# Performance work log

Hardware: AMD Instinct MI355X
Metric: run time of the kernel (lower is better)

Reference implementation:

```python
import jax, jax.numpy as jnp
import numpy as np

B, T, C, H, K = 4, 2048, 2048, 32, 64
CHUNK = 64  # matches `splits = 64` in the torch source
EPS = 0.00064


def setup_inputs() -> dict:
    key = jax.random.key(0)
    ks = jax.random.split(key, 16)
    return {
        "x": jax.random.normal(ks[0], (B, T, C), jnp.float32),
        "state": jax.random.normal(ks[1], (1, 1, C), jnp.float32) * 0.1,
        "wkvstate": jax.random.normal(ks[2], (H, K, K), jnp.float32) * 0.02,
        "time_mix_k": jax.random.uniform(ks[3], (1, 1, C), jnp.float32),
        "time_mix_v": jax.random.uniform(ks[4], (1, 1, C), jnp.float32),
        "time_mix_r": jax.random.uniform(ks[5], (1, 1, C), jnp.float32),
        "time_mix_g": jax.random.uniform(ks[6], (1, 1, C), jnp.float32),
        "time_decay": jax.random.normal(ks[7], (H, K), jnp.float32) * 0.5,
        "time_faaaa": jax.random.normal(ks[8], (H, K), jnp.float32) * 0.1,
        "w_r": jax.random.normal(ks[9], (C, C), jnp.float32) * 0.02,
        "w_k": jax.random.normal(ks[10], (C, C), jnp.float32) * 0.02,
        "w_v": jax.random.normal(ks[11], (C, C), jnp.float32) * 0.02,
        "w_g": jax.random.normal(ks[12], (C, C), jnp.float32) * 0.02,
        "w_o": jax.random.normal(ks[13], (C, C), jnp.float32) * 0.02,
        "ln_w": jnp.ones((C,), jnp.float32),
        "ln_b": jnp.zeros((C,), jnp.float32),
    }


def reference(x, state, wkvstate, time_mix_k, time_mix_v, time_mix_r, time_mix_g,
              time_decay, time_faaaa, w_r, w_k, w_v, w_g, w_o, ln_w, ln_b):
    Bx, Tx, Cx = x.shape
    Hx, Kx = time_decay.shape

    # TimeShift (training path): prepend learned state, drop last token
    xx = jnp.concatenate([jnp.broadcast_to(state, (Bx, 1, Cx)), x[:, :-1]], axis=1)
    xk = x * time_mix_k + xx * (1.0 - time_mix_k)
    xv = x * time_mix_v + xx * (1.0 - time_mix_v)
    xr = x * time_mix_r + xx * (1.0 - time_mix_r)
    xg = x * time_mix_g + xx * (1.0 - time_mix_g)

    g = jax.nn.silu(xg @ w_g.T)  # (B,T,C)

    def to_heads(t):  # (B,T,C) -> (B,H,T,K)
        return t.reshape(Bx, Tx, Hx, Kx).transpose(0, 2, 1, 3)

    r = to_heads(xr @ w_r.T)
    k = to_heads(xk @ w_k.T)
    v = to_heads(xv @ w_v.T)

    w = jnp.exp(-jnp.exp(time_decay))  # (H,K), per-channel decay in (0,1)
    t_idx = jnp.arange(Tx)
    wfor = w[None, :, None, :] ** t_idx[None, None, :, None]          # w^t
    wback = w[None, :, None, :] ** (Tx - 1 - t_idx)[None, None, :, None]  # w^(T-1-t)

    # contribution of the incoming wkv state: (r * w^t) @ S0
    base = jnp.einsum('bhtk,hkj->bhtj', r * wfor, wkvstate)
    # bonus (u) diagonal term: sum_k(k_t * u * r_t) * v_t
    base = base + jnp.sum(k * r * time_faaaa[None, :, None, :], axis=-1, keepdims=True) * v

    kw = k * wback  # k_t scaled by w^(T-1-t), as in the source

    # strict-past causal product on shifted slices (r[:,1:] vs kw/v[:,:-1]),
    # computed chunk-by-chunk exactly like the blocked tril loop.
    rr, kk, vv = r[:, :, 1:], kw[:, :, :-1], v[:, :, :-1]
    Tm = Tx - 1
    pad = (-Tm) % CHUNK
    pd = lambda a: jnp.pad(a, ((0, 0), (0, 0), (0, pad), (0, 0)))
    rr, kk, vv = pd(rr), pd(kk), pd(vv)
    nC = (Tm + pad) // CHUNK
    resh = lambda a: a.reshape(Bx, Hx, nC, CHUNK, Kx).transpose(2, 0, 1, 3, 4)
    rc_, kc_, vc_ = resh(rr), resh(kk), resh(vv)
    mask = jnp.tril(jnp.ones((CHUNK, CHUNK), bool))  # q <= p (inclusive) == tril(i-j) globally

    def step(S, inp):
        rc, kc, vc = inp  # (B,H,CHUNK,K)
        att = jnp.einsum('bhpk,bhqk->bhpq', rc, kc)
        att = jnp.where(mask, att, 0.0)
        out = jnp.einsum('bhpq,bhqk->bhpk', att, vc) + jnp.einsum('bhpk,bhkj->bhpj', rc, S)
        S = S + jnp.einsum('bhqk,bhqj->bhkj', kc, vc)
        return S, out

    S0 = jnp.zeros((Bx, Hx, Kx, Kx), x.dtype)
    _, outs = jax.lax.scan(step, S0, (rc_, kc_, vc_))  # (nC,B,H,CHUNK,K)
    intra = outs.transpose(1, 2, 0, 3, 4).reshape(Bx, Hx, nC * CHUNK, Kx)[:, :, :Tm]
    wkv = base.at[:, :, 1:].add(intra)  # (B,H,T,K)

    # GroupNorm(n_head groups) after a bf16 round-trip, as in the source
    y = wkv.transpose(0, 2, 1, 3)  # (B,T,H,K)
    y = y.astype(jnp.bfloat16).astype(jnp.float32)
    mu = jnp.mean(y, axis=-1, keepdims=True)
    var = jnp.var(y, axis=-1, keepdims=True)
    y = (y - mu) / jnp.sqrt(var + EPS)
    y = y * ln_w.reshape(Hx, Kx) + ln_b.reshape(Hx, Kx)
    y = y.reshape(Bx, Tx, Cx)

    return (y * g) @ w_o.T
```

## Files before the change

kernel.cpp:

```cpp
#include <hip/hip_runtime.h>

#define Bn 4
#define Tn 2048
#define Cn 2048
#define Hn 32
#define Mn 8192
#define EPSV 0.00064f
#define SEGS 8
#define ZTHR 96.f

typedef __attribute__((ext_vector_type(4))) float f32x4;
typedef _Float16 half4 __attribute__((ext_vector_type(4)));
typedef _Float16 half8 __attribute__((ext_vector_type(8)));

__device__ __forceinline__ unsigned short f2bf(float f) {
  unsigned int u = __float_as_uint(f);
  u += 0x7fffu + ((u >> 16) & 1u);
  return (unsigned short)(u >> 16);
}
__device__ __forceinline__ float bf2f(unsigned short h) {
  return __uint_as_float(((unsigned int)h) << 16);
}

__global__ __launch_bounds__(256) void wcast_f16_kernel(
    const float* __restrict__ src, _Float16* __restrict__ dst) {
  const size_t e = ((size_t)blockIdx.x * 256 + threadIdx.x) * 4;
  const float4 v = *(const float4*)(src + e);
  half4 h;
  h.x = (_Float16)v.x; h.y = (_Float16)v.y; h.z = (_Float16)v.z; h.w = (_Float16)v.w;
  *(half4*)(dst + e) = h;
}

__global__ __launch_bounds__(256) void mix_one_kernel(
    const float* __restrict__ x, const float* __restrict__ state,
    const float* __restrict__ tm, _Float16* __restrict__ xm) {
  const size_t e = ((size_t)blockIdx.x * 256 + threadIdx.x) * 4;
  const int c = (int)(e & (Cn - 1));
  const int t = (int)((e >> 11) & (Tn - 1));
  float4 xv  = *(const float4*)(x + e);
  float4 xxv = (t == 0) ? *(const float4*)(state + c) : *(const float4*)(x + e - Cn);
  float4 m = *(const float4*)(tm + c);
  half4 o;
  o.x = (_Float16)(xv.x * m.x + xxv.x * (1.f - m.x));
  o.y = (_Float16)(xv.y * m.y + xxv.y * (1.f - m.y));
  o.z = (_Float16)(xv.z * m.z + xxv.z * (1.f - m.z));
  o.w = (_Float16)(xv.w * m.w + xxv.w * (1.f - m.w));
  *(half4*)(xm + e) = o;
}

template <int OUT_F16>
__global__ __launch_bounds__(512, 2) void gemm256_kernel(
    const _Float16* __restrict__ A, const _Float16* __restrict__ W,
    void* __restrict__ Ov) {
  __shared__ _Float16 As[2][256 * 64];
  __shared__ _Float16 Bs[2][256 * 64];
  const int tid = threadIdx.x;
  const int wid = tid >> 6, ln = tid & 63;
  const int wm = wid >> 2, wn = wid & 3;
  const int m16 = ln & 15, qd = ln >> 4;

  const int mtile = blockIdx.y, ntile = blockIdx.x;
  const _Float16* Ab = A + (size_t)mtile * 256 * Cn;
  const _Float16* Wb = W + (size_t)ntile * 256 * Cn;

  const _Float16* gA[4]; const _Float16* gB[4];
  int lof[4];
#pragma unroll
  for (int i = 0; i < 4; ++i) {
    int r = ((wid * 4 + i) << 3) + (ln >> 3);
    int q = (ln & 7) ^ (r & 7);
    gA[i] = Ab + (size_t)r * Cn + (q << 3);
    gB[i] = Wb + (size_t)r * Cn + (q << 3);
    lof[i] = ((wid * 4 + i) << 10);
  }
  int aob[2], bob[2];
#pragma unroll
  for (int h = 0; h < 2; ++h) {
    int sl = ((h << 2) + qd) ^ (m16 & 7);
    aob[h] = (wm * 128 + m16) * 128 + sl * 16;
    bob[h] = (wn * 64 + m16) * 128 + sl * 16;
  }

  f32x4 acc[8][4];
#pragma unroll
  for (int i = 0; i < 8; ++i)
#pragma unroll
    for (int j = 0; j < 4; ++j) acc[i][j] = 0.f;

#pragma unroll
  for (int i = 0; i < 4; ++i) {
    __builtin_amdgcn_global_load_lds(
        (const __attribute__((address_space(1))) void*)(gA[i]),
        (__attribute__((address_space(3))) void*)((char*)&As[0][0] + lof[i]), 16, 0, 0);
    __builtin_amdgcn_global_load_lds(
        (const __attribute__((address_space(1))) void*)(gB[i]),
        (__attribute__((address_space(3))) void*)((char*)&Bs[0][0] + lof[i]), 16, 0, 0);
  }

  const int NT = Cn / 64;
  for (int t = 0; t < NT; ++t) {
    const int b = t & 1;
    if (t + 1 < NT) {
      const int k0 = (t + 1) << 6;
#pragma unroll
      for (int i = 0; i < 4; ++i) {
        __builtin_amdgcn_global_load_lds(
            (const __attribute__((address_space(1))) void*)(gA[i] + k0),
            (__attribute__((address_space(3))) void*)((char*)&As[b ^ 1][0] + lof[i]), 16, 0, 0);
        __builtin_amdgcn_global_load_lds(
            (const __attribute__((address_space(1))) void*)(gB[i] + k0),
            (__attribute__((address_space(3))) void*)((char*)&Bs[b ^ 1][0] + lof[i]), 16, 0, 0);
      }
      asm volatile("s_waitcnt vmcnt(8)" ::: "memory");
    } else {
      asm volatile("s_waitcnt vmcnt(0)" ::: "memory");
    }
    __builtin_amdgcn_s_barrier();

    const char* Abase = (const char*)&As[b][0];
    const char* Bbase = (const char*)&Bs[b][0];
    half8 bf[4][2];
#pragma unroll
    for (int nf = 0; nf < 4; ++nf)
#pragma unroll
      for (int h = 0; h < 2; ++h)
        bf[nf][h] = *(const half8*)(Bbase + nf * 2048 + bob[h]);
#pragma unroll
    for (int p = 0; p < 4; ++p) {
      half8 af[2][2];
#pragma unroll
      for (int sub = 0; sub < 2; ++sub)
#pragma unroll
        for (int h = 0; h < 2; ++h)
          af[sub][h] = *(const half8*)(Abase + (p * 2 + sub) * 2048 + aob[h]);
      __builtin_amdgcn_s_setprio(1);
#pragma unroll
      for (int sub = 0; sub < 2; ++sub)
#pragma unroll
        for (int nf = 0; nf < 4; ++nf) {
          acc[p * 2 + sub][nf] =
              __builtin_amdgcn_mfma_f32_16x16x32_f16(af[sub][0], bf[nf][0], acc[p * 2 + sub][nf], 0, 0, 0);
          acc[p * 2 + sub][nf] =
              __builtin_amdgcn_mfma_f32_16x16x32_f16(af[sub][1], bf[nf][1], acc[p * 2 + sub][nf], 0, 0, 0);
        }
      __builtin_amdgcn_s_setprio(0);
    }
    __builtin_amdgcn_s_barrier();
  }

  const size_t obase = (size_t)mtile * 256 * Cn + (size_t)ntile * 256;
#pragma unroll
  for (int fr = 0; fr < 8; ++fr) {
#pragma unroll
    for (int nf = 0; nf < 4; ++nf) {
      int col  = wn * 64 + nf * 16 + m16;
      int row0 = wm * 128 + fr * 16 + (qd << 2);
      f32x4 cv = acc[fr][nf];
      if constexpr (OUT_F16) {
        _Float16* Ob = (_Float16*)Ov + obase;
#pragma unroll
        for (int rg = 0; rg < 4; ++rg)
          Ob[(size_t)(row0 + rg) * Cn + col] = (_Float16)cv[rg];
      } else {
        float* Ob = (float*)Ov + obase;
#pragma unroll
        for (int rg = 0; rg < 4; ++rg)
          Ob[(size_t)(row0 + rg) * Cn + col] = cv[rg];
      }
    }
  }
}

__global__ __launch_bounds__(256) void seg_sum_kernel(
    const _Float16* __restrict__ kA, const _Float16* __restrict__ vA,
    const float* __restrict__ td, float* __restrict__ segsum) {
  __shared__ float sK[32][68];
  __shared__ float sV[32][68];
  __shared__ float sEw[64];
  __shared__ float sEwMin;
  const int tid = threadIdx.x;
  const int bh = blockIdx.x;
  const int seg = SEGS - 1 - blockIdx.y;
  const int b = bh >> 5, h = bh & 31;
  const size_t colbase = (size_t)b * Tn * Cn + h * 64;
  const _Float16* kG = kA + colbase;
  const _Float16* vG = vA + colbase;

  if (tid < 64) sEw[tid] = __expf(td[h * 64 + tid]);
  __syncthreads();
  if (tid == 0) {
    float mn = sEw[0];
    for (int i = 1; i < 64; ++i) mn = fminf(mn, sEw[i]);
    sEwMin = mn;
  }
  __syncthreads();

  const int uk0 = (tid >> 4) << 2;
  const int uj0 = (tid & 15) << 2;
  float su[16];
#pragma unroll
  for (int i = 0; i < 16; ++i) su[i] = 0.f;

  const int c0 = seg * (64 / SEGS), c1 = c0 + (64 / SEGS);
  for (int c = c0; c < c1; ++c) {
    const int tb = c << 5;
    if ((float)(Tn - 32 - tb) * sEwMin >= ZTHR) continue;
#pragma unroll
    for (int rep = 0; rep < 2; ++rep) {
      int f4 = tid + (rep << 8);
      int row = f4 >> 4;
      int col = (f4 & 15) << 2;
      int t = tb + row;
      size_t off = (size_t)t * Cn + col;
      half4 ku = *(const half4*)(kG + off);
      half4 vu = *(const half4*)(vG + off);
      float4 vf; vf.x = (float)vu.x; vf.y = (float)vu.y; vf.z = (float)vu.z; vf.w = (float)vu.w;
      *(float4*)&sV[row][col] = vf;
      float e = (float)(Tn - 1 - t);
      float4 kw;
      kw.x = (float)ku.x * __expf(-e * sEw[col + 0]);
      kw.y = (float)ku.y * __expf(-e * sEw[col + 1]);
      kw.z = (float)ku.z * __expf(-e * sEw[col + 2]);
      kw.w = (float)ku.w * __expf(-e * sEw[col + 3]);
      *(float4*)&sK[row][col] = kw;
    }
    __syncthreads();
    for (int q = 0; q < 32; ++q) {
      float4 kq = *(const float4*)&sK[q][uk0];
      float4 vq = *(const float4*)&sV[q][uj0];
      su[0]  += kq.x * vq.x; su[1]  += kq.x * vq.y; su[2]  += kq.x * vq.z; su[3]  += kq.x * vq.w;
      su[4]  += kq.y * vq.x; su[5]  += kq.y * vq.y; su[6]  += kq.y * vq.z; su[7]  += kq.y * vq.w;
      su[8]  += kq.z * vq.x; su[9]  += kq.z * vq.y; su[10] += kq.z * vq.z; su[11] += kq.z * vq.w;
      su[12] += kq.w * vq.x; su[13] += kq.w * vq.y; su[14] += kq.w * vq.z; su[15] += kq.w * vq.w;
    }
    __syncthreads();
  }
  float* dst = segsum + ((size_t)bh * SEGS + seg) * 4096;
#pragma unroll
  for (int i = 0; i < 4; ++i) {
    float4 s; s.x = su[i * 4 + 0]; s.y = su[i * 4 + 1]; s.z = su[i * 4 + 2]; s.w = su[i * 4 + 3];
    *(float4*)(dst + (uk0 + i) * 64 + uj0) = s;
  }
}

__global__ __launch_bounds__(256) void scan_kernel(
    const _Float16* __restrict__ rA, const _Float16* __restrict__ kA,
    const _Float16* __restrict__ vA, const _Float16* __restrict__ gA,
    const float* __restrict__ wkvst, const float* __restrict__ td,
    const float* __restrict__ faaaa, const float* __restrict__ lnw,
    const float* __restrict__ lnb, const float* __restrict__ segsum,
    _Float16* __restrict__ A2) {
  __shared__ float sR[32][68];
  __shared__ float sK[32][68];
  __shared__ float sV[32][68];
  __shared__ float sRW[32][68];
  __shared__ float sS[64][68];
  __shared__ float sS0[64][68];
  __shared__ float sAtt[32][36];
  __shared__ float sEw[64];
  __shared__ float sU[64];
  __shared__ float sDotP[32][16];
  __shared__ float sRedM[32][8];
  __shared__ float sRedQ[32][8];
  __shared__ float sMV[32][2];
  __shared__ float sEwMin;
  const int tid = threadIdx.x;
  const int bh = blockIdx.x;
  const int seg = SEGS - 1 - blockIdx.y;
  const int b = bh >> 5, h = bh & 31;
  const size_t colbase = (size_t)b * Tn * Cn + h * 64;
  const _Float16* rG = rA + colbase;
  const _Float16* kG = kA + colbase;
  const _Float16* vG = vA + colbase;
  const _Float16* gG = gA + colbase;
  _Float16* outG = A2 + colbase;

  if (tid < 64) {
    sEw[tid] = __expf(td[h * 64 + tid]);
    sU[tid]  = faaaa[h * 64 + tid];
  }
  {
    float4 acc4[4];
#pragma unroll
    for (int j = 0; j < 4; ++j) { acc4[j].x = 0.f; acc4[j].y = 0.f; acc4[j].z = 0.f; acc4[j].w = 0.f; }
    for (int sp = 0; sp < seg; ++sp) {
      const float* basep = segsum + ((size_t)bh * SEGS + sp) * 4096;
#pragma unroll
      for (int j = 0; j < 4; ++j) {
        int f4 = tid + j * 256;
        int row = f4 >> 4, c4 = (f4 & 15) << 2;
        float4 m = *(const float4*)(basep + row * 64 + c4);
        acc4[j].x += m.x; acc4[j].y += m.y; acc4[j].z += m.z; acc4[j].w += m.w;
      }
    }
#pragma unroll
    for (int j = 0; j < 4; ++j) {
      int f4 = tid + j * 256;
      int row = f4 >> 4, c4 = (f4 & 15) << 2;
      *(float4*)&sS[row][c4] = acc4[j];
      *(float4*)&sS0[row][c4] = *(const float4*)(wkvst + (size_t)h * 4096 + row * 64 + c4);
    }
  }
  __syncthreads();
  if (tid == 0) {
    float mn = sEw[0];
    for (int i = 1; i < 64; ++i) mn = fminf(mn, sEw[i]);
    sEwMin = mn;
  }
  __syncthreads();

  const int ap  = tid >> 3;
  const int aq0 = (tid & 7) << 2;
  const int oj0 = (tid & 7) << 3;
  const int uk0 = (tid >> 4) << 2;
  const int uj0 = (tid & 15) << 2;
  float lw[8], lb[8];
#pragma unroll
  for (int i = 0; i < 8; ++i) { lw[i] = lnw[h * 64 + oj0 + i]; lb[i] = lnb[h * 64 + oj0 + i]; }

  bool snz = (seg > 0) && ((float)(Tn - seg * 256) * sEwMin < ZTHR);

  const int c0 = seg * (64 / SEGS), c1 = c0 + (64 / SEGS);
  for (int c = c0; c < c1; ++c) {
    const int tb = c << 5;
    const bool skipc  = ((float)(Tn - 32 - tb) * sEwMin) >= ZTHR;
    const bool active = ((float)tb * sEwMin) < 88.f;
#pragma unroll
    for (int rep = 0; rep < 2; ++rep) {
      int f4 = tid + (rep << 8);
      int row = f4 >> 4;
      int col = (f4 & 15) << 2;
      int t = tb + row;
      size_t off = (size_t)t * Cn + col;
      half4 ru = *(const half4*)(rG + off);
      half4 ku = *(const half4*)(kG + off);
      half4 vu = *(const half4*)(vG + off);
      float4 rv; rv.x = (float)ru.x; rv.y = (float)ru.y; rv.z = (float)ru.z; rv.w = (float)ru.w;
      float4 kf; kf.x = (float)ku.x; kf.y = (float)ku.y; kf.z = (float)ku.z; kf.w = (float)ku.w;
      float4 vf; vf.x = (float)vu.x; vf.y = (float)vu.y; vf.z = (float)vu.z; vf.w = (float)vu.w;
      *(float4*)&sV[row][col] = vf;
      sDotP[row][f4 & 15] =
          kf.x * rv.x * sU[col + 0] + kf.y * rv.y * sU[col + 1] +
          kf.z * rv.z * sU[col + 2] + kf.w * rv.w * sU[col + 3];
      if (!skipc) {
        *(float4*)&sR[row][col] = rv;
        float e = (float)(Tn - 1 - t);
        float4 kw;
        kw.x = kf.x * __expf(-e * sEw[col + 0]); kw.y = kf.y * __expf(-e * sEw[col + 1]);
        kw.z = kf.z * __expf(-e * sEw[col + 2]); kw.w = kf.w * __expf(-e * sEw[col + 3]);
        *(float4*)&sK[row][col] = kw;
      }
      if (active) {
        float tt = (float)t;
        float4 rw;
        rw.x = rv.x * __expf(-tt * sEw[col + 0]); rw.y = rv.y * __expf(-tt * sEw[col + 1]);
        rw.z = rv.z * __expf(-tt * sEw[col + 2]); rw.w = rv.w * __expf(-tt * sEw[col + 3]);
        *(float4*)&sRW[row][col] = rw;
      }
    }
    __syncthreads();
    if (!skipc) {
      float a[4] = {0.f, 0.f, 0.f, 0.f};
      for (int k = 0; k < 64; k += 4) {
        float4 rv = *(const float4*)&sR[ap][k];
#pragma unroll
        for (int qq = 0; qq < 4; ++qq) {
          float4 kv = *(const float4*)&sK[aq0 + qq][k];
          a[qq] += rv.x * kv.x + rv.y * kv.y + rv.z * kv.z + rv.w * kv.w;
        }
      }
#pragma unroll
      for (int qq = 0; qq < 4; ++qq)
        sAtt[ap][aq0 + qq] = ((aq0 + qq) < ap) ? a[qq] : 0.f;
      __syncthreads();
    }
    float y[8];
    {
      float o[8];
#pragma unroll
      for (int i = 0; i < 8; ++i) o[i] = 0.f;
      if (!skipc) {
        for (int q = 0; q < 32; ++q) {
          float aw = sAtt[ap][q];
          float4 v0 = *(const float4*)&sV[q][oj0];
          float4 v1 = *(const float4*)&sV[q][oj0 + 4];
          o[0] += aw * v0.x; o[1] += aw * v0.y; o[2] += aw * v0.z; o[3] += aw * v0.w;
          o[4] += aw * v1.x; o[5] += aw * v1.y; o[6] += aw * v1.z; o[7] += aw * v1.w;
        }
      }
      if (snz) {
        for (int k = 0; k < 64; ++k) {
          float rw = sR[ap][k];
          float4 s0 = *(const float4*)&sS[k][oj0];
          float4 s1 = *(const float4*)&sS[k][oj0 + 4];
          o[0] += rw * s0.x; o[1] += rw * s0.y; o[2] += rw * s0.z; o[3] += rw * s0.w;
          o[4] += rw * s1.x; o[5] += rw * s1.y; o[6] += rw * s1.z; o[7] += rw * s1.w;
        }
      }
      if (active) {
        for (int k = 0; k < 64; ++k) {
          float rw = sRW[ap][k];
          float4 s0 = *(const float4*)&sS0[k][oj0];
          float4 s1 = *(const float4*)&sS0[k][oj0 + 4];
          o[0] += rw * s0.x; o[1] += rw * s0.y; o[2] += rw * s0.z; o[3] += rw * s0.w;
          o[4] += rw * s1.x; o[5] += rw * s1.y; o[6] += rw * s1.z; o[7] += rw * s1.w;
        }
      }
      float dot = 0.f;
#pragma unroll
      for (int s = 0; s < 16; ++s) dot += sDotP[ap][s];
#pragma unroll
      for (int i = 0; i < 8; ++i) o[i] += dot * sV[ap][oj0 + i];
      float sm = 0.f, sq = 0.f;
#pragma unroll
      for (int i = 0; i < 8; ++i) {
        y[i] = bf2f(f2bf(o[i]));
        sm += y[i]; sq += y[i] * y[i];
      }
      sRedM[ap][tid & 7] = sm; sRedQ[ap][tid & 7] = sq;
    }
    __syncthreads();
    if ((tid & 7) == 0) {
      float sm = 0.f, sq = 0.f;
#pragma unroll
      for (int i = 0; i < 8; ++i) { sm += sRedM[ap][i]; sq += sRedQ[ap][i]; }
      float mu = sm * (1.f / 64.f);
      float var = sq * (1.f / 64.f) - mu * mu;
      sMV[ap][0] = mu; sMV[ap][1] = rsqrtf(var + EPSV);
    }
    __syncthreads();
    {
      float mu = sMV[ap][0], rs = sMV[ap][1];
      int t = tb + ap;
      size_t off = (size_t)t * Cn + oj0;
      half4 g0 = *(const half4*)(gG + off);
      half4 g1 = *(const half4*)(gG + off + 4);
      float gv[8] = {(float)g0.x, (float)g0.y, (float)g0.z, (float)g0.w,
                     (float)g1.x, (float)g1.y, (float)g1.z, (float)g1.w};
      _Float16 us[8];
#pragma unroll
      for (int i = 0; i < 8; ++i) {
        float yn = (y[i] - mu) * rs * lw[i] + lb[i];
        float gs = gv[i] / (1.f + __expf(-gv[i]));
        us[i] = (_Float16)(yn * gs);
      }
      half4 o0, o1;
      o0.x = us[0]; o0.y = us[1]; o0.z = us[2]; o0.w = us[3];
      o1.x = us[4]; o1.y = us[5]; o1.z = us[6]; o1.w = us[7];
      *(half4*)(outG + off) = o0;
      *(half4*)(outG + off + 4) = o1;
    }
    if (!skipc) {
      float su[16];
#pragma unroll
      for (int i = 0; i < 4; ++i) {
        float4 s = *(const float4*)&sS[uk0 + i][uj0];
        su[i * 4 + 0] = s.x; su[i * 4 + 1] = s.y; su[i * 4 + 2] = s.z; su[i * 4 + 3] = s.w;
      }
      for (int q = 0; q < 32; ++q) {
        float4 kq = *(const float4*)&sK[q][uk0];
        float4 vq = *(const float4*)&sV[q][uj0];
        su[0]  += kq.x * vq.x; su[1]  += kq.x * vq.y; su[2]  += kq.x * vq.z; su[3]  += kq.x * vq.w;
        su[4]  += kq.y * vq.x; su[5]  += kq.y * vq.y; su[6]  += kq.y * vq.z; su[7]  += kq.y * vq.w;
        su[8]  += kq.z * vq.x; su[9]  += kq.z * vq.y; su[10] += kq.z * vq.z; su[11] += kq.z * vq.w;
        su[12] += kq.w * vq.x; su[13] += kq.w * vq.y; su[14] += kq.w * vq.z; su[15] += kq.w * vq.w;
      }
#pragma unroll
      for (int i = 0; i < 4; ++i) {
        float4 s; s.x = su[i * 4 + 0]; s.y = su[i * 4 + 1]; s.z = su[i * 4 + 2]; s.w = su[i * 4 + 3];
        *(float4*)&sS[uk0 + i][uj0] = s;
      }
      snz = true;
      __syncthreads();
    }
  }
}

extern "C" void kernel_launch(void* const* d_in, const int* in_sizes, int n_in,
                              void* d_out, int out_size, void* d_ws, size_t ws_size,
                              hipStream_t stream) {
  const float* x     = (const float*)d_in[0];
  const float* state = (const float*)d_in[1];
  const float* wkvst = (const float*)d_in[2];
  const float* tmk   = (const float*)d_in[3];
  const float* tmv   = (const float*)d_in[4];
  const float* tmr   = (const float*)d_in[5];
  const float* tmg   = (const float*)d_in[6];
  const float* td    = (const float*)d_in[7];
  const float* faaaa = (const float*)d_in[8];
  const float* w_r   = (const float*)d_in[9];
  const float* w_k   = (const float*)d_in[10];
  const float* w_v   = (const float*)d_in[11];
  const float* w_g   = (const float*)d_in[12];
  const float* w_o   = (const float*)d_in[13];
  const float* ln_w  = (const float*)d_in[14];
  const float* ln_b  = (const float*)d_in[15];
  float* out = (float*)d_out;
  char* ws = (char*)d_ws;

  _Float16* wh  = (_Float16*)(ws);
  _Float16* xm  = (_Float16*)(ws + 16777216);
  _Float16* A2  = (_Float16*)(ws + 16777216);
  _Float16* proj = (_Float16*)(ws + 50331648);
  float* segsum  = (float*)(ws + 184549376);
  const size_t SLOT_E = (size_t)Mn * Cn;
  _Float16* R = proj;
  _Float16* K = proj + SLOT_E;
  _Float16* V = proj + 2 * SLOT_E;
  _Float16* G = proj + 3 * SLOT_E;

  const float* tms[4]  = {tmr, tmk, tmv, tmg};
  const float* wsrc[4] = {w_r, w_k, w_v, w_g};
  _Float16*    pdst[4] = {R, K, V, G};

  for (int s = 0; s < 4; ++s) {
    wcast_f16_kernel<<<dim3(4096), 256, 0, stream>>>(wsrc[s], wh);
    mix_one_kernel<<<dim3(16384), 256, 0, stream>>>(x, state, tms[s], xm);
    gemm256_kernel<1><<<dim3(Cn / 256, Mn / 256), 512, 0, stream>>>(xm, wh, pdst[s]);
  }

  seg_sum_kernel<<<dim3(128, SEGS), 256, 0, stream>>>(K, V, td, segsum);
  scan_kernel<<<dim3(128, SEGS), 256, 0, stream>>>(R, K, V, G, wkvst, td, faaaa,
                                                   ln_w, ln_b, segsum, A2);

  wcast_f16_kernel<<<dim3(4096), 256, 0, stream>>>(w_o, wh);
  gemm256_kernel<0><<<dim3(Cn / 256, Mn / 256), 512, 0, stream>>>(A2, wh, out);

  (void)in_sizes; (void)n_in; (void)out_size; (void)ws_size;
}
```

Baseline: 769.1 us.

## Fuse token-mix into one pass and store scan tiles in swizzled fp16 LDS

The four separate mix kernels become one kernel that reads x once and writes all four mixed inputs, with workspace buffers rotated so each GEMM writes over the previous input slot. The scan kernel now keeps R, K, V, RW and the initial state in fp16 shared memory with an XOR swizzle and loads 8-wide half vectors. Its dot products use fdot2 when available. This is meant to cut repeated global reads of x and to lower LDS footprint and bandwidth in the scan. In exchange, the decayed keys and the initial state are rounded to fp16, which may cost accuracy.

```diff
diff --git a/kernel.cpp b/kernel.cpp
--- a/kernel.cpp
+++ b/kernel.cpp
@@ -12,6 +12,18 @@
 typedef __attribute__((ext_vector_type(4))) float f32x4;
 typedef _Float16 half4 __attribute__((ext_vector_type(4)));
 typedef _Float16 half8 __attribute__((ext_vector_type(8)));
+typedef _Float16 h2 __attribute__((ext_vector_type(2)));
+
+#if defined(__has_builtin)
+#if __has_builtin(__builtin_amdgcn_fdot2)
+#define HAS_FDOT2 1
+#endif
+#endif
+#ifndef HAS_FDOT2
+#define HAS_FDOT2 0
+#endif
+
+#define SWZ(row, col) ((col) ^ ((((row) >> 2) & 7) << 3))
 
 __device__ __forceinline__ unsigned short f2bf(float f) {
   unsigned int u = __float_as_uint(f);
@@ -20,6 +32,23 @@
 }
 __device__ __forceinline__ float bf2f(unsigned short h) {
   return __uint_as_float(((unsigned int)h) << 16);
+}
+
+__device__ __forceinline__ float dot8(half8 a, half8 b, float acc) {
+#if HAS_FDOT2
+  acc = __builtin_amdgcn_fdot2(__builtin_shufflevector(a, a, 0, 1),
+                               __builtin_shufflevector(b, b, 0, 1), acc, false);
+  acc = __builtin_amdgcn_fdot2(__builtin_shufflevector(a, a, 2, 3),
+                               __builtin_shufflevector(b, b, 2, 3), acc, false);
+  acc = __builtin_amdgcn_fdot2(__builtin_shufflevector(a, a, 4, 5),
+                               __builtin_shufflevector(b, b, 4, 5), acc, false);
+  acc = __builtin_amdgcn_fdot2(__builtin_shufflevector(a, a, 6, 7),
+                               __builtin_shufflevector(b, b, 6, 7), acc, false);
+#else
+#pragma unroll
+  for (int i = 0; i < 8; ++i) acc += (float)a[i] * (float)b[i];
+#endif
+  return acc;
 }
 
 __global__ __launch_bounds__(256) void wcast_f16_kernel(
@@ -31,21 +60,30 @@
   *(half4*)(dst + e) = h;
 }
 
-__global__ __launch_bounds__(256) void mix_one_kernel(
+__global__ __launch_bounds__(256) void mix4_kernel(
     const float* __restrict__ x, const float* __restrict__ state,
-    const float* __restrict__ tm, _Float16* __restrict__ xm) {
+    const float* __restrict__ tmr, const float* __restrict__ tmk,
+    const float* __restrict__ tmv, const float* __restrict__ tmg,
+    _Float16* __restrict__ xr, _Float16* __restrict__ xk,
+    _Float16* __restrict__ xv, _Float16* __restrict__ xg) {
   const size_t e = ((size_t)blockIdx.x * 256 + threadIdx.x) * 4;
   const int c = (int)(e & (Cn - 1));
   const int t = (int)((e >> 11) & (Tn - 1));
-  float4 xv  = *(const float4*)(x + e);
-  float4 xxv = (t == 0) ? *(const float4*)(state + c) : *(const float4*)(x + e - Cn);
-  float4 m = *(const float4*)(tm + c);
-  half4 o;
-  o.x = (_Float16)(xv.x * m.x + xxv.x * (1.f - m.x));
-  o.y = (_Float16)(xv.y * m.y + xxv.y * (1.f - m.y));
-  o.z = (_Float16)(xv.z * m.z + xxv.z * (1.f - m.z));
-  o.w = (_Float16)(xv.w * m.w + xxv.w * (1.f - m.w));
-  *(half4*)(xm + e) = o;
+  float4 xv_ = *(const float4*)(x + e);
+  float4 xx  = (t == 0) ? *(const float4*)(state + c) : *(const float4*)(x + e - Cn);
+  float4 dx; dx.x = xv_.x - xx.x; dx.y = xv_.y - xx.y; dx.z = xv_.z - xx.z; dx.w = xv_.w - xx.w;
+  const float* tms[4] = {tmr, tmk, tmv, tmg};
+  _Float16* dsts[4] = {xr, xk, xv, xg};
+#pragma unroll
+  for (int s = 0; s < 4; ++s) {
+    float4 m = *(const float4*)(tms[s] + c);
+    half4 o;
+    o.x = (_Float16)(xx.x + dx.x * m.x);
+    o.y = (_Float16)(xx.y + dx.y * m.y);
+    o.z = (_Float16)(xx.z + dx.z * m.z);
+    o.w = (_Float16)(xx.w + dx.w * m.w);
+    *(half4*)(dsts[s] + e) = o;
+  }
 }
 
 template <int OUT_F16>
@@ -119,12 +157,12 @@
 
     const char* Abase = (const char*)&As[b][0];
     const char* Bbase = (const char*)&Bs[b][0];
-    half8 bf[4][2];
+    half8 bfr[4][2];
 #pragma unroll
     for (int nf = 0; nf < 4; ++nf)
 #pragma unroll
       for (int h = 0; h < 2; ++h)
-        bf[nf][h] = *(const half8*)(Bbase + nf * 2048 + bob[h]);
+        bfr[nf][h] = *(const half8*)(Bbase + nf * 2048 + bob[h]);
 #pragma unroll
     for (int p = 0; p < 4; ++p) {
       half8 af[2][2];
@@ -139,9 +177,9 @@
 #pragma unroll
         for (int nf = 0; nf < 4; ++nf) {
           acc[p * 2 + sub][nf] =
-              __builtin_amdgcn_mfma_f32_16x16x32_f16(af[sub][0], bf[nf][0], acc[p * 2 + sub][nf], 0, 0, 0);
+              __builtin_amdgcn_mfma_f32_16x16x32_f16(af[sub][0], bfr[nf][0], acc[p * 2 + sub][nf], 0, 0, 0);
           acc[p * 2 + sub][nf] =
-              __builtin_amdgcn_mfma_f32_16x16x32_f16(af[sub][1], bf[nf][1], acc[p * 2 + sub][nf], 0, 0, 0);
+              __builtin_amdgcn_mfma_f32_16x16x32_f16(af[sub][1], bfr[nf][1], acc[p * 2 + sub][nf], 0, 0, 0);
         }
       __builtin_amdgcn_s_setprio(0);
     }
@@ -250,16 +288,16 @@
     const float* __restrict__ faaaa, const float* __restrict__ lnw,
     const float* __restrict__ lnb, const float* __restrict__ segsum,
     _Float16* __restrict__ A2) {
-  __shared__ float sR[32][68];
-  __shared__ float sK[32][68];
-  __shared__ float sV[32][68];
-  __shared__ float sRW[32][68];
+  __shared__ __align__(16) _Float16 sR[32][72];
+  __shared__ __align__(16) _Float16 sK[32][72];
+  __shared__ __align__(16) _Float16 sV[32][72];
+  __shared__ __align__(16) _Float16 sRW[32][72];
+  __shared__ __align__(16) _Float16 sS0[64][72];
   __shared__ float sS[64][68];
-  __shared__ float sS0[64][68];
   __shared__ float sAtt[32][36];
   __shared__ float sEw[64];
   __shared__ float sU[64];
-  __shared__ float sDotP[32][16];
+  __shared__ float sDotP[32][8];
   __shared__ float sRedM[32][8];
   __shared__ float sRedQ[32][8];
   __shared__ float sMV[32][2];
@@ -298,8 +336,20 @@
       int f4 = tid + j * 256;
       int row = f4 >> 4, c4 = (f4 & 15) << 2;
       *(float4*)&sS[row][c4] = acc4[j];
-      *(float4*)&sS0[row][c4] = *(const float4*)(wkvst + (size_t)h * 4096 + row * 64 + c4);
-    }
+    }
+    int row = tid >> 2, c0 = (tid & 3) << 4;
+    const float* sp = wkvst + (size_t)h * 4096 + row * 64 + c0;
+    float4 f0 = *(const float4*)(sp);
+    float4 f1 = *(const float4*)(sp + 4);
+    float4 f2 = *(const float4*)(sp + 8);
+    float4 f3 = *(const float4*)(sp + 12);
+    half8 h0, h1;
+    h0[0] = (_Float16)f0.x; h0[1] = (_Float16)f0.y; h0[2] = (_Float16)f0.z; h0[3] = (_Float16)f0.w;
+    h0[4] = (_Float16)f1.x; h0[5] = (_Float16)f1.y; h0[6] = (_Float16)f1.z; h0[7] = (_Float16)f1.w;
+    h1[0] = (_Float16)f2.x; h1[1] = (_Float16)f2.y; h1[2] = (_Float16)f2.z; h1[3] = (_Float16)f2.w;
+    h1[4] = (_Float16)f3.x; h1[5] = (_Float16)f3.y; h1[6] = (_Float16)f3.z; h1[7] = (_Float16)f3.w;
+    *(half8*)&sS0[row][SWZ(row, c0)] = h0;
+    *(half8*)&sS0[row][SWZ(row, c0 + 8)] = h1;
   }
   __syncthreads();
   if (tid == 0) {
@@ -314,6 +364,8 @@
   const int oj0 = (tid & 7) << 3;
   const int uk0 = (tid >> 4) << 2;
   const int uj0 = (tid & 15) << 2;
+  const int srow = tid >> 3;
+  const int scol = (tid & 7) << 3;
   float lw[8], lb[8];
 #pragma unroll
   for (int i = 0; i < 8; ++i) { lw[i] = lnw[h * 64 + oj0 + i]; lb[i] = lnb[h * 64 + oj0 + i]; }
@@ -325,53 +377,50 @@
     const int tb = c << 5;
     const bool skipc  = ((float)(Tn - 32 - tb) * sEwMin) >= ZTHR;
     const bool active = ((float)tb * sEwMin) < 88.f;
-#pragma unroll
-    for (int rep = 0; rep < 2; ++rep) {
-      int f4 = tid + (rep << 8);
-      int row = f4 >> 4;
-      int col = (f4 & 15) << 2;
-      int t = tb + row;
-      size_t off = (size_t)t * Cn + col;
-      half4 ru = *(const half4*)(rG + off);
-      half4 ku = *(const half4*)(kG + off);
-      half4 vu = *(const half4*)(vG + off);
-      float4 rv; rv.x = (float)ru.x; rv.y = (float)ru.y; rv.z = (float)ru.z; rv.w = (float)ru.w;
-      float4 kf; kf.x = (float)ku.x; kf.y = (float)ku.y; kf.z = (float)ku.z; kf.w = (float)ku.w;
-      float4 vf; vf.x = (float)vu.x; vf.y = (float)vu.y; vf.z = (float)vu.z; vf.w = (float)vu.w;
-      *(float4*)&sV[row][col] = vf;
-      sDotP[row][f4 & 15] =
-          kf.x * rv.x * sU[col + 0] + kf.y * rv.y * sU[col + 1] +
-          kf.z * rv.z * sU[col + 2] + kf.w * rv.w * sU[col + 3];
+    {
+      int t = tb + srow;
+      size_t off = (size_t)t * Cn + scol;
+      half8 ru = *(const half8*)(rG + off);
+      half8 ku = *(const half8*)(kG + off);
+      half8 vu = *(const half8*)(vG + off);
+      *(half8*)&sV[srow][SWZ(srow, scol)] = vu;
+      float dp = 0.f;
+#pragma unroll
+      for (int i = 0; i < 8; ++i) dp += (float)ku[i] * (float)ru[i] * sU[scol + i];
+      sDotP[srow][tid & 7] = dp;
       if (!skipc) {
-        *(float4*)&sR[row][col] = rv;
+        *(half8*)&sR[srow][SWZ(srow, scol)] = ru;
         float e = (float)(Tn - 1 - t);
-        float4 kw;
-        kw.x = kf.x * __expf(-e * sEw[col + 0]); kw.y = kf.y * __expf(-e * sEw[col + 1]);
-        kw.z = kf.z * __expf(-e * sEw[col + 2]); kw.w = kf.w * __expf(-e * sEw[col + 3]);
-        *(float4*)&sK[row][col] = kw;
+        half8 kwh;
+#pragma unroll
+        for (int i = 0; i < 8; ++i)
+          kwh[i] = (_Float16)((float)ku[i] * __expf(-e * sEw[scol + i]));
+        *(half8*)&sK[srow][SWZ(srow, scol)] = kwh;
       }
       if (active) {
         float tt = (float)t;
-        float4 rw;
-        rw.x = rv.x * __expf(-tt * sEw[col + 0]); rw.y = rv.y * __expf(-tt * sEw[col + 1]);
-        rw.z = rv.z * __expf(-tt * sEw[col + 2]); rw.w = rv.w * __expf(-tt * sEw[col + 3]);
-        *(float4*)&sRW[row][col] = rw;
+        half8 rwh;
+#pragma unroll
+        for (int i = 0; i < 8; ++i)
+          rwh[i] = (_Float16)((float)ru[i] * __expf(-tt * sEw[scol + i]));
+        *(half8*)&sRW[srow][SWZ(srow, scol)] = rwh;
       }
     }
     __syncthreads();
     if (!skipc) {
-      float a[4] = {0.f, 0.f, 0.f, 0.f};
-      for (int k = 0; k < 64; k += 4) {
-        float4 rv = *(const float4*)&sR[ap][k];
+      float a4[4] = {0.f, 0.f, 0.f, 0.f};
+      for (int k = 0; k < 64; k += 8) {
+        half8 rv = *(const half8*)&sR[ap][SWZ(ap, k)];
 #pragma unroll
         for (int qq = 0; qq < 4; ++qq) {
-          float4 kv = *(const float4*)&sK[aq0 + qq][k];
-          a[qq] += rv.x * kv.x + rv.y * kv.y + rv.z * kv.z + rv.w * kv.w;
+          int row = aq0 + qq;
+          half8 kv = *(const half8*)&sK[row][SWZ(row, k)];
+          a4[qq] = dot8(rv, kv, a4[qq]);
         }
       }
 #pragma unroll
       for (int qq = 0; qq < 4; ++qq)
-        sAtt[ap][aq0 + qq] = ((aq0 + qq) < ap) ? a[qq] : 0.f;
+        sAtt[ap][aq0 + qq] = ((aq0 + qq) < ap) ? a4[qq] : 0.f;
       __syncthreads();
     }
     float y[8];
@@ -382,35 +431,44 @@
       if (!skipc) {
         for (int q = 0; q < 32; ++q) {
           float aw = sAtt[ap][q];
-          float4 v0 = *(const float4*)&sV[q][oj0];
-          float4 v1 = *(const float4*)&sV[q][oj0 + 4];
-          o[0] += aw * v0.x; o[1] += aw * v0.y; o[2] += aw * v0.z; o[3] += aw * v0.w;
-          o[4] += aw * v1.x; o[5] += aw * v1.y; o[6] += aw * v1.z; o[7] += aw * v1.w;
+          half8 vv = *(const half8*)&sV[q][SWZ(q, oj0)];
+#pragma unroll
+          for (int i = 0; i < 8; ++i) o[i] += aw * (float)vv[i];
         }
       }
       if (snz) {
-        for (int k = 0; k < 64; ++k) {
-          float rw = sR[ap][k];
-          float4 s0 = *(const float4*)&sS[k][oj0];
-          float4 s1 = *(const float4*)&sS[k][oj0 + 4];
-          o[0] += rw * s0.x; o[1] += rw * s0.y; o[2] += rw * s0.z; o[3] += rw * s0.w;
-          o[4] += rw * s1.x; o[5] += rw * s1.y; o[6] += rw * s1.z; o[7] += rw * s1.w;
+        for (int k8 = 0; k8 < 64; k8 += 8) {
+          half8 rv = *(const half8*)&sR[ap][SWZ(ap, k8)];
+#pragma unroll
+          for (int kk = 0; kk < 8; ++kk) {
+            float rw = (float)rv[kk];
+            const float* srow_ = &sS[k8 + kk][oj0];
+            float4 s0 = *(const float4*)(srow_);
+            float4 s1 = *(const float4*)(srow_ + 4);
+            o[0] += rw * s0.x; o[1] += rw * s0.y; o[2] += rw * s0.z; o[3] += rw * s0.w;
+            o[4] += rw * s1.x; o[5] += rw * s1.y; o[6] += rw * s1.z; o[7] += rw * s1.w;
+          }
         }
       }
       if (active) {
-        for (int k = 0; k < 64; ++k) {
-          float rw = sRW[ap][k];
-          float4 s0 = *(const float4*)&sS0[k][oj0];
-          float4 s1 = *(const float4*)&sS0[k][oj0 + 4];
-          o[0] += rw * s0.x; o[1] += rw * s0.y; o[2] += rw * s0.z; o[3] += rw * s0.w;
-          o[4] += rw * s1.x; o[5] += rw * s1.y; o[6] += rw * s1.z; o[7] += rw * s1.w;
+        for (int k8 = 0; k8 < 64; k8 += 8) {
+          half8 rv = *(const half8*)&sRW[ap][SWZ(ap, k8)];
+#pragma unroll
+          for (int kk = 0; kk < 8; ++kk) {
+            float rw = (float)rv[kk];
+            int k = k8 + kk;
+            half8 s08 = *(const half8*)&sS0[k][SWZ(k, oj0)];
+#pragma unroll
+            for (int i = 0; i < 8; ++i) o[i] += rw * (float)s08[i];
+          }
         }
       }
       float dot = 0.f;
 #pragma unroll
-      for (int s = 0; s < 16; ++s) dot += sDotP[ap][s];
-#pragma unroll
-      for (int i = 0; i < 8; ++i) o[i] += dot * sV[ap][oj0 + i];
+      for (int s = 0; s < 8; ++s) dot += sDotP[ap][s];
+      half8 vme = *(const half8*)&sV[ap][SWZ(ap, oj0)];
+#pragma unroll
+      for (int i = 0; i < 8; ++i) o[i] += dot * (float)vme[i];
       float sm = 0.f, sq = 0.f;
 #pragma unroll
       for (int i = 0; i < 8; ++i) {
@@ -433,22 +491,16 @@
       float mu = sMV[ap][0], rs = sMV[ap][1];
       int t = tb + ap;
       size_t off = (size_t)t * Cn + oj0;
-      half4 g0 = *(const half4*)(gG + off);
-      half4 g1 = *(const half4*)(gG + off + 4);
-      float gv[8] = {(float)g0.x, (float)g0.y, (float)g0.z, (float)g0.w,
-                     (float)g1.x, (float)g1.y, (float)g1.z, (float)g1.w};
-      _Float16 us[8];
+      half8 g8 = *(const half8*)(gG + off);
+      half8 o8;
 #pragma unroll
       for (int i = 0; i < 8; ++i) {
+        float gv = (float)g8[i];
         float yn = (y[i] - mu) * rs * lw[i] + lb[i];
-        float gs = gv[i] / (1.f + __expf(-gv[i]));
-        us[i] = (_Float16)(yn * gs);
-      }
-      half4 o0, o1;
-      o0.x = us[0]; o0.y = us[1]; o0.z = us[2]; o0.w = us[3];
-      o1.x = us[4]; o1.y = us[5]; o1.z = us[6]; o1.w = us[7];
-      *(half4*)(outG + off) = o0;
-      *(half4*)(outG + off + 4) = o1;
+        float gs = gv / (1.f + __expf(-gv));
+        o8[i] = (_Float16)(yn * gs);
+      }
+      *(half8*)(outG + off) = o8;
     }
     if (!skipc) {
       float su[16];
@@ -458,12 +510,14 @@
         su[i * 4 + 0] = s.x; su[i * 4 + 1] = s.y; su[i * 4 + 2] = s.z; su[i * 4 + 3] = s.w;
       }
       for (int q = 0; q < 32; ++q) {
-        float4 kq = *(const float4*)&sK[q][uk0];
-        float4 vq = *(const float4*)&sV[q][uj0];
-        su[0]  += kq.x * vq.x; su[1]  += kq.x * vq.y; su[2]  += kq.x * vq.z; su[3]  += kq.x * vq.w;
-        su[4]  += kq.y * vq.x; su[5]  += kq.y * vq.y; su[6]  += kq.y * vq.z; su[7]  += kq.y * vq.w;
-        su[8]  += kq.z * vq.x; su[9]  += kq.z * vq.y; su[10] += kq.z * vq.z; su[11] += kq.z * vq.w;
-        su[12] += kq.w * vq.x; su[13] += kq.w * vq.y; su[14] += kq.w * vq.z; su[15] += kq.w * vq.w;
+        half4 kq4 = *(const half4*)&sK[q][SWZ(q, uk0)];
+        half4 vq4 = *(const half4*)&sV[q][SWZ(q, uj0)];
+        float kx = (float)kq4.x, ky = (float)kq4.y, kz = (float)kq4.z, kw_ = (float)kq4.w;
+        float vx = (float)vq4.x, vy = (float)vq4.y, vz = (float)vq4.z, vw = (float)vq4.w;
+        su[0]  += kx * vx; su[1]  += kx * vy; su[2]  += kx * vz; su[3]  += kx * vw;
+        su[4]  += ky * vx; su[5]  += ky * vy; su[6]  += ky * vz; su[7]  += ky * vw;
+        su[8]  += kz * vx; su[9]  += kz * vy; su[10] += kz * vz; su[11] += kz * vw;
+        su[12] += kw_ * vx; su[13] += kw_ * vy; su[14] += kw_ * vz; su[15] += kw_ * vw;
       }
 #pragma unroll
       for (int i = 0; i < 4; ++i) {
@@ -498,26 +552,30 @@
   float* out = (float*)d_out;
   char* ws = (char*)d_ws;
 
-  _Float16* wh  = (_Float16*)(ws);
-  _Float16* xm  = (_Float16*)(ws + 16777216);
-  _Float16* A2  = (_Float16*)(ws + 16777216);
-  _Float16* proj = (_Float16*)(ws + 50331648);
+  const size_t SLOT = 33554432;
+  _Float16* wh   = (_Float16*)(ws);
+  _Float16* M0   = (_Float16*)(ws + 16777216);
+  _Float16* M1   = (_Float16*)(ws + 16777216 + SLOT);
+  _Float16* M2   = (_Float16*)(ws + 16777216 + 2 * SLOT);
+  _Float16* M3   = (_Float16*)(ws + 16777216 + 3 * SLOT);
+  _Float16* Rbuf = (_Float16*)(ws + 16777216 + 4 * SLOT);
   float* segsum  = (float*)(ws + 184549376);
-  const size_t SLOT_E = (size_t)Mn * Cn;
-  _Float16* R = proj;
-  _Float16* K = proj + SLOT_E;
-  _Float16* V = proj + 2 * SLOT_E;
-  _Float16* G = proj + 3 * SLOT_E;
-
-  const float* tms[4]  = {tmr, tmk, tmv, tmg};
+
+  mix4_kernel<<<dim3(16384), 256, 0, stream>>>(x, state, tmr, tmk, tmv, tmg, M0, M1, M2, M3);
+
   const float* wsrc[4] = {w_r, w_k, w_v, w_g};
-  _Float16*    pdst[4] = {R, K, V, G};
+  const _Float16* asrc[4] = {M0, M1, M2, M3};
+  _Float16* pdst[4] = {Rbuf, M0, M1, M2};
 
   for (int s = 0; s < 4; ++s) {
     wcast_f16_kernel<<<dim3(4096), 256, 0, stream>>>(wsrc[s], wh);
-    mix_one_kernel<<<dim3(16384), 256, 0, stream>>>(x, state, tms[s], xm);
-    gemm256_kernel<1><<<dim3(Cn / 256, Mn / 256), 512, 0, stream>>>(xm, wh, pdst[s]);
-  }
+    gemm256_kernel<1><<<dim3(Cn / 256, Mn / 256), 512, 0, stream>>>(asrc[s], wh, pdst[s]);
+  }
+  _Float16* R = Rbuf;
+  _Float16* K = M0;
+  _Float16* V = M1;
+  _Float16* G = M2;
+  _Float16* A2 = M3;
 
   seg_sum_kernel<<<dim3(128, SEGS), 256, 0, stream>>>(K, V, td, segsum);
   scan_kernel<<<dim3(128, SEGS), 256, 0, stream>>>(R, K, V, G, wkvst, td, faaaa,
```

After: 730.3 us. 1.05x faster.
